# Kernel optimization log

Hardware: AMD Instinct MI355X
Metric: run time of the kernel (lower is better)

The kernel has to match this reference:

```python
import jax, jax.numpy as jnp
import numpy as np

B, T, N = 16, 16, 1024          # patients, max visits, code_num
C, G, H, A, P = 48, 32, 150, 32, 32  # code_size, graph_size, hidden_size, t_attention_size, pool attn size
OUT = 1
NEG = -1e30


def setup_inputs() -> dict:
    key = jax.random.key(0)
    ks = jax.random.split(key, 20)
    code_x = (jax.random.uniform(ks[0], (B, T, N)) < 0.2).astype(jnp.float32)
    neighbors = (jax.random.uniform(ks[1], (B, T, N)) < 0.2).astype(jnp.float32)
    cat = jax.random.randint(ks[2], (B, T, N), 0, 8)
    # divided[..., 0/1/2] = disjoint m1 (persistent) / m2 (emerging-neighbor) / m3 (emerging-unrelated) masks
    divided = jnp.stack([(cat == 0), (cat == 1), (cat == 2)], axis=-1).astype(jnp.int32)
    lens = jax.random.randint(ks[3], (B,), 1, T + 1)
    prior = jax.random.uniform(ks[4], (N,))
    adj = (jax.random.uniform(ks[5], (N, N)) * (jax.random.uniform(ks[6], (N, N)) < 0.05)).astype(jnp.float32)

    def nrm(k, shape, scale=0.05):
        return (jax.random.normal(k, shape) * scale).astype(jnp.float32)

    return dict(
        code_x=code_x, divided=divided, neighbors=neighbors, lens=lens, prior=prior, adj=adj,
        c_emb=nrm(ks[7], (N, C)), n_emb=nrm(ks[8], (N, C)), u_emb=nrm(ks[9], (N, G)),
        Wg=nrm(ks[10], (C, G)), bg=jnp.zeros((G,), jnp.float32),
        W_ih=nrm(ks[11], (3 * H, G)), b_ih=jnp.zeros((3 * H,), jnp.float32),
        W_hh=nrm(ks[12], (3 * H, H)), b_hh=jnp.zeros((3 * H,), jnp.float32),
        Wq=nrm(ks[13], (G, A)), bq=jnp.zeros((A,), jnp.float32),
        Wk=nrm(ks[14], (G, A)), bk=jnp.zeros((A,), jnp.float32),
        Wv=nrm(ks[15], (G, H)), bv=jnp.zeros((H,), jnp.float32),
        Wp=nrm(ks[16], (H, P)), bp=jnp.zeros((P,), jnp.float32),
        ctx=nrm(ks[17], (P,)),
        Wc=nrm(ks[18], (H, OUT)), bc=jnp.zeros((OUT,), jnp.float32),
    )


def _forward(code_x, divided, neighbors, lens, prior, adj, c_emb, n_emb, u_emb,
             Wg, bg, W_ih, b_ih, W_hh, b_hh, Wq, bq, Wk, bk, Wv, bv,
             Wp, bp, ctx, Wc, bc):
    pr = prior[:, None]                                  # [N,1] disease prior scaling of graph messages
    scale = 1.0 / jnp.sqrt(jnp.asarray(A, jnp.float32))

    def gru(x, h):
        # torch nn.GRUCell semantics; x: [B,N,G], h: [B,N,H]
        gi = jnp.einsum('bng,kg->bnk', x, W_ih) + b_ih
        gh = jnp.einsum('bnh,kh->bnk', h, W_hh) + b_hh
        ir, iz, i_n = jnp.split(gi, 3, -1)
        hr, hz, h_n = jnp.split(gh, 3, -1)
        r = jax.nn.sigmoid(ir + hr)
        z = jax.nn.sigmoid(iz + hz)
        cand = jnp.tanh(i_n + r * h_n)
        return (1.0 - z) * cand + z * h

    def step(carry, xs):
        h_prev, no_prev, t = carry
        cx, nb, dv = xs                                  # [B,N], [B,N], [B,N,3]
        c = cx[..., None]
        n = nb[..., None]
        # --- GraphLayer: adjacency message passing, prior-weighted ---
        ce = c * c_emb                                   # [B,N,C]
        ne = n * n_emb
        agg_c = jnp.einsum('mn,bnc->bmc', adj, ce) * pr
        agg_n = jnp.einsum('mn,bnc->bmc', adj, ne) * pr
        co = jax.nn.leaky_relu((ce + c * (agg_c + agg_n)) @ Wg + bg)   # [B,N,G]
        no = jax.nn.leaky_relu((ne + n * (agg_n + agg_c)) @ Wg + bg)
        # --- TransitionLayer ---
        m1 = dv[..., 0] > 0
        m2 = dv[..., 1] > 0
        m3 = dv[..., 2] > 0
        m23 = m2 | m3
        h_gru = gru(co, h_prev)                          # GRU branch for persistent codes (m1)
        # attention branch: queries = prev-step neighbor embeddings (m2) or unrelated embeddings (m3)
        qf = jnp.where(m2[..., None], no_prev, 0.0) + jnp.where(m3[..., None], u_emb, 0.0)
        q = qf @ Wq + bq
        k = co @ Wk + bk
        v = co @ Wv + bv                                 # [B,N,H]
        g = jnp.einsum('bma,bna->bmn', q, k) * scale     # scores over active m2|m3 keys only
        g = jnp.where(m23[:, None, :], g, NEG)
        h_att = jnp.tanh(jnp.einsum('bmn,bnh->bmh', jax.nn.softmax(g, axis=-1), v))
        t_pos = (t > 0).astype(co.dtype)                 # m23 branch only runs for t > 0 (as in original)
        h_new = jnp.where(m1[..., None], h_gru, 0.0) + t_pos * jnp.where(m23[..., None], h_att, 0.0)
        # masked maxes (0 when the index set is empty, as in original)
        om1 = jnp.max(jnp.where(m1[..., None], h_gru, NEG), axis=1)
        om1 = jnp.where(jnp.any(m1, axis=1)[:, None], om1, 0.0)
        om23 = jnp.max(jnp.where(m23[..., None], h_att, NEG), axis=1)
        om23 = jnp.where(jnp.any(m23, axis=1)[:, None], om23, 0.0)
        out_t = om1 + t_pos * om23                       # [B,H]
        return (h_new, no, t + 1), out_t

    h0 = jnp.zeros((B, N, H), jnp.float32)
    no0 = jnp.zeros((B, N, G), jnp.float32)
    xs = (jnp.transpose(code_x, (1, 0, 2)),
          jnp.transpose(neighbors, (1, 0, 2)),
          jnp.transpose(divided, (1, 0, 2, 3)))
    _, outs = jax.lax.scan(step, (h0, no0, jnp.int32(0)), xs)
    outs = jnp.transpose(outs, (1, 0, 2))                # [B,T,H]
    # --- DotProductAttention pooling over valid (ragged) timesteps ---
    vu = (outs @ Wp + bp) @ ctx                          # [B,T]
    valid = jnp.arange(T)[None, :] < lens[:, None]
    score = jax.nn.softmax(jnp.where(valid, vu, NEG), axis=-1)
    pooled = jnp.sum(outs * score[..., None], axis=1)    # [B,H]
    # --- Classifier (dropout identity at eval, activation=None) ---
    return pooled @ Wc + bc


def reference(code_x, divided, neighbors, lens, prior, adj, c_emb, n_emb, u_emb,
              Wg, bg, W_ih, b_ih, W_hh, b_hh, Wq, bq, Wk, bk, Wv, bv,
              Wp, bp, ctx, Wc, bc):
    return _forward(code_x, divided, neighbors, lens, prior, adj, c_emb, n_emb, u_emb,
                    Wg, bg, W_ih, b_ih, W_hh, b_hh, Wq, bq, Wk, bk, Wv, bv,
                    Wp, bp, ctx, Wc, bc)
```

## Files before the change

kernel.cpp:

```cpp
#include <hip/hip_runtime.h>

#define B_ 16
#define T_ 16
#define N_ 1024
#define C_ 48
#define G_ 32
#define H_ 150
#define A_ 32
#define P_ 32
#define H3_ 450
#define NNZ_CAP 262144
#define CAP1 256
#define CAP23 384
#define CHCAP 40960
#define CHCAPL 16384
#define SCALE_ 0.17677669529663687f

__device__ __forceinline__ unsigned fenc(float f){
  unsigned u = __float_as_uint(f);
  return (u & 0x80000000u) ? ~u : (u | 0x80000000u);
}
__device__ __forceinline__ float fdec(unsigned e){
  unsigned u = (e & 0x80000000u) ? (e & 0x7fffffffu) : ~e;
  return __uint_as_float(u);
}
__device__ __forceinline__ float sigmf(float x){ return 1.f/(1.f+__expf(-x)); }
__device__ __forceinline__ float wmaxf(float v){
  #pragma unroll
  for (int d=32; d>0; d>>=1) v = fmaxf(v, __shfl_xor(v,d));
  return v;
}

#define FMA16(W, PTR, ACC) do { \
    const float4* _c4 = (const float4*)(PTR); \
    float4 _c0=_c4[0], _c1=_c4[1], _c2=_c4[2], _c3=_c4[3]; \
    ACC[0]=fmaf((W),_c0.x,ACC[0]); ACC[1]=fmaf((W),_c0.y,ACC[1]); \
    ACC[2]=fmaf((W),_c0.z,ACC[2]); ACC[3]=fmaf((W),_c0.w,ACC[3]); \
    ACC[4]=fmaf((W),_c1.x,ACC[4]); ACC[5]=fmaf((W),_c1.y,ACC[5]); \
    ACC[6]=fmaf((W),_c1.z,ACC[6]); ACC[7]=fmaf((W),_c1.w,ACC[7]); \
    ACC[8]=fmaf((W),_c2.x,ACC[8]); ACC[9]=fmaf((W),_c2.y,ACC[9]); \
    ACC[10]=fmaf((W),_c2.z,ACC[10]); ACC[11]=fmaf((W),_c2.w,ACC[11]); \
    ACC[12]=fmaf((W),_c3.x,ACC[12]); ACC[13]=fmaf((W),_c3.y,ACC[13]); \
    ACC[14]=fmaf((W),_c3.z,ACC[14]); ACC[15]=fmaf((W),_c3.w,ACC[15]); \
  } while(0)

__global__ void k_csr_cnt(const float* __restrict__ adj, int* __restrict__ rcnt){
  int m = blockIdx.x; int tid = threadIdx.x;
  int c = 0;
  for (int n = tid; n < N_; n += 256) c += (adj[(size_t)m*N_+n] != 0.f) ? 1 : 0;
  __shared__ int sr[256];
  sr[tid]=c; __syncthreads();
  for (int s=128; s>0; s>>=1){ if (tid<s) sr[tid]+=sr[tid+s]; __syncthreads(); }
  if (tid==0) rcnt[m]=sr[0];
}
__global__ void k_csr_scan(const int* __restrict__ rcnt, int* __restrict__ rowptr){
  int lane = threadIdx.x;
  int s = 0;
  for (int r=0;r<16;++r) s += rcnt[lane*16+r];
  int incl = s;
  for (int d=1; d<64; d<<=1){ int y = __shfl_up(incl, d); if (lane>=d) incl += y; }
  int run = incl - s;
  for (int r=0;r<16;++r){ rowptr[lane*16+r] = run; run += rcnt[lane*16+r]; }
  if (lane==63) rowptr[N_] = incl;
}
__global__ void k_csr_fill(const float* __restrict__ adj, const float* __restrict__ prior,
                           const int* __restrict__ rowptr,
                           int* __restrict__ ccol, float* __restrict__ cval){
  int m = blockIdx.x; int lane = threadIdx.x;
  int base = rowptr[m];
  float pm = prior[m];
  for (int it=0; it<N_/64; ++it){
    int n = it*64+lane;
    float a = adj[(size_t)m*N_+n];
    bool pnz = (a != 0.f);
    unsigned long long mk = __ballot(pnz);
    if (pnz){
      int idx = base + __popcll(mk & ((1ULL<<lane)-1ULL));
      if (idx < NNZ_CAP){ ccol[idx]=n; cval[idx]=a*pm; }
    }
    base += __popcll(mk);
  }
}

__global__ void k_masks(const int* __restrict__ divided, int* __restrict__ lst23,
                        int* __restrict__ pos1,
                        int* __restrict__ cnt23, int* __restrict__ cnt1){
  int bt = blockIdx.x; int lane = threadIdx.x;
  int base23=0, base1=0;
  for (int it=0; it<N_/64; ++it){
    int n = it*64+lane;
    const int* dv = &divided[((size_t)bt*N_+n)*3];
    int d0=dv[0], d1=dv[1], d2=dv[2];
    bool p23 = (d1>0)||(d2>0); bool p1 = d0>0;
    unsigned long long mk23 = __ballot(p23);
    unsigned long long mk1  = __ballot(p1);
    unsigned long long ltm = (1ULL<<lane)-1ULL;
    if (p23){ int idx = base23 + __popcll(mk23 & ltm); lst23[(size_t)bt*N_+idx]=n; }
    if (p1){ int idx = base1 + __popcll(mk1 & ltm); pos1[(size_t)bt*N_+n]=idx; }
    base23 += __popcll(mk23); base1 += __popcll(mk1);
  }
  if (lane==0){ cnt23[bt]=base23; cnt1[bt]=base1; }
}

__global__ void k_chains(const int* __restrict__ divided,
                         unsigned* __restrict__ chN, int* __restrict__ nchN,
                         unsigned* __restrict__ chH, int* __restrict__ nchH,
                         unsigned* __restrict__ chL, int* __restrict__ nchL){
  int idx = blockIdx.x*256 + threadIdx.x;
  if (idx >= B_*N_) return;
  int b = idx >> 10, n = idx & (N_-1);
  unsigned m1m = 0;
  for (int t=0;t<T_;++t){
    int d0 = divided[(((size_t)(b*T_+t))*N_ + n)*3];
    if (d0>0) m1m |= (1u<<t);
  }
  unsigned heads = m1m & ~(m1m<<1);
  while (heads){
    int t0 = __builtin_ctz(heads); heads &= (heads-1u);
    unsigned run = m1m >> t0;
    int len = __builtin_ctz(~run);
    unsigned enc = ((unsigned)b<<18)|((unsigned)n<<8)|((unsigned)t0<<4)|(unsigned)(len-1);
    int f = 0;
    if (t0 >= 2){
      size_t pidx = ((size_t)(b*T_+t0-1)*N_ + n)*3;
      if ((divided[pidx+1] | divided[pidx+2]) > 0) f = 1;
    }
    if (f){ int i2 = atomicAdd(nchH,1); if (i2 < CHCAP) chH[i2]=enc; }
    else  { int i2 = atomicAdd(nchN,1); if (i2 < CHCAP) chN[i2]=enc; }
    if (len >= 2){
      int i2 = atomicAdd(nchL, 1);
      if (i2 < CHCAPL) chL[i2] = enc;
    }
  }
}

__global__ void k_wt(const float* __restrict__ W_ih, const float* __restrict__ W_hh,
                     const float* __restrict__ Wq, const float* __restrict__ bq,
                     const float* __restrict__ Wk,
                     float* __restrict__ WihT, float* __restrict__ WhhT,
                     float* __restrict__ Md){
  int idx = blockIdx.x*256+threadIdx.x;
  if (idx < G_*H3_){ int g=idx/H3_, k=idx-g*H3_; WihT[g*H3_+k]=W_ih[(size_t)k*G_+g]; }
  int idx2 = idx - G_*H3_;
  if (idx2>=0 && idx2 < H_*H3_){ int h=idx2/H3_, k=idx2-h*H3_; WhhT[h*H3_+k]=W_hh[(size_t)k*H_+h]; }
  int e = idx - (G_*H3_ + H_*H3_);
  if (e>=0 && e<1024){
    int g=e>>5, gp=e&31;
    float acc=0.f;
    #pragma unroll
    for (int a=0;a<A_;++a) acc = fmaf(Wq[g*A_+a], Wk[gp*A_+a], acc);
    Md[e]=acc;
  }
  int e2 = e - 1024;
  if (e2>=0 && e2<32){
    float acc=0.f;
    #pragma unroll
    for (int a=0;a<A_;++a) acc = fmaf(Wk[e2*A_+a], bq[a], acc);
    Md[1024+e2]=acc;
  }
}

__global__ void k_init(float* __restrict__ om23f, int* __restrict__ nchN,
                       int* __restrict__ nchH, int* __restrict__ nchL){
  int i = blockIdx.x*256+threadIdx.x;
  if (i<B_*T_*H_){ om23f[i]=0.f; }
  if (i==0){ *nchN = 0; *nchH = 0; *nchL = 0; }
}

__global__ __launch_bounds__(256) void k_cono(
    const float* __restrict__ code_x, const float* __restrict__ neighbors,
    const int* __restrict__ divided,
    const int* __restrict__ rowptr, const int* __restrict__ ccol, const float* __restrict__ cval,
    const float* __restrict__ c_emb, const float* __restrict__ n_emb,
    const float* __restrict__ Wg, const float* __restrict__ bg,
    float* __restrict__ co, float* __restrict__ no_)
{
  __shared__ float sCo[4][C_], sNo[4][C_];
  int w = threadIdx.x >> 6, lane = threadIdx.x & 63;
  int gw = blockIdx.x*4 + w;
  int bt = gw >> 10, m = gw & (N_-1);
  int t = bt & (T_-1);
  const int* dv = &divided[(size_t)gw*3];
  int d0=dv[0], d1=dv[1], d2=dv[2];
  bool needCo = (d0|d1|d2) > 0;
  bool needNo = (t < T_-1) && (divided[((size_t)(gw+N_))*3+1] > 0);
  if (!needCo && !needNo) return;
  float cxm = code_x[gw], nbm = neighbors[gw];
  float acc = 0.f;
  bool needAcc = (needCo && cxm!=0.f) || (needNo && nbm!=0.f);
  if (needAcc){
    int s = rowptr[m], e = rowptr[m+1];
    if (s > NNZ_CAP) s = NNZ_CAP;
    if (e > NNZ_CAP) e = NNZ_CAP;
    int btN = bt << 10;
    for (int base = s; base < e; base += 64){
      int j = base + lane;
      int cc = 0; float wx = 0.f, wy = 0.f;
      if (j < e){
        cc = ccol[j];
        float cv = cval[j];
        float xs = code_x[btN+cc], ys = neighbors[btN+cc];
        wx = cv*xs; wy = cv*ys;
      }
      unsigned long long mk = __ballot(wx!=0.f || wy!=0.f);
      while (mk){
        int u0 = __builtin_ctzll(mk); mk &= (mk-1ULL);
        int u1 = -1;
        if (mk){ u1 = __builtin_ctzll(mk); mk &= (mk-1ULL); }
        int u1s = (u1>=0)? u1 : u0;
        int n0 = __shfl(cc,u0); float a0x=__shfl(wx,u0), a0y=__shfl(wy,u0);
        int n1 = __shfl(cc,u1s); float a1x=__shfl(wx,u1s), a1y=__shfl(wy,u1s);
        float ce0=0.f,ne0=0.f,ce1=0.f,ne1=0.f;
        if (lane < C_){
          ce0 = c_emb[(size_t)n0*C_+lane]; ne0 = n_emb[(size_t)n0*C_+lane];
          ce1 = c_emb[(size_t)n1*C_+lane]; ne1 = n_emb[(size_t)n1*C_+lane];
        }
        acc = fmaf(a0x, ce0, acc); acc = fmaf(a0y, ne0, acc);
        if (u1>=0){ acc = fmaf(a1x, ce1, acc); acc = fmaf(a1y, ne1, acc); }
      }
    }
  }
  if (lane < C_){
    sCo[w][lane] = cxm * (c_emb[(size_t)m*C_+lane] + acc);
    sNo[w][lane] = nbm * (n_emb[(size_t)m*C_+lane] + acc);
  }
  asm volatile("s_waitcnt lgkmcnt(0)" ::: "memory");
  int g = lane & 31; bool isNo = lane >= 32;
  const float* src = isNo ? sNo[w] : sCo[w];
  float a2 = bg[g];
  #pragma unroll
  for (int c=0;c<C_;++c) a2 = fmaf(src[c], Wg[c*G_+g], a2);
  float r = a2 >= 0.f ? a2 : 0.01f*a2;
  if (isNo ? needNo : needCo){
    float* dst = isNo ? no_ : co;
    dst[(size_t)gw*G_ + g] = r;
  }
}

__global__ __launch_bounds__(384) void k_attn(
    const float* __restrict__ co, const float* __restrict__ no_,
    const float* __restrict__ u_emb, const int* __restrict__ divided,
    const int* __restrict__ lst23, const int* __restrict__ cnt23, const int* __restrict__ pos1,
    const float* __restrict__ Md, const float* __restrict__ Wv, const float* __restrict__ bv,
    float* __restrict__ hsel, float* __restrict__ om23f)
{
  int b = blockIdx.x; int t = blockIdx.y + 1; int bt = b*T_ + t;
  int cnt = cnt23[bt]; if (cnt > CAP23) cnt = CAP23;
  if (cnt == 0) return;
  __shared__ int   sLst[CAP23];
  __shared__ __align__(16) float sCo[CAP23][G_];
  __shared__ __align__(16) float sW[G_*H_ + H_ + 8];
  __shared__ unsigned sMax[H_];
  int tid = threadIdx.x; int lane = tid & 63;
  for (int i=tid; i<cnt; i+=384) sLst[i] = lst23[(size_t)bt*N_+i];
  for (int i=tid; i<1056; i+=384) sW[i] = Md[i];
  unsigned sent = fenc(-1e30f);
  for (int i=tid; i<H_; i+=384) sMax[i] = sent;
  __syncthreads();
  for (int i=tid; i<cnt*8; i+=384){
    int rrow = i>>3, seg = i&7;
    float4 v = *(const float4*)&co[((((size_t)bt<<10) + sLst[rrow])<<5) + seg*4];
    *(float4*)&sCo[rrow][seg*4] = v;
  }
  bool act = (tid < cnt);
  int n = 0;
  float qpp[G_];
  if (act){
    n = sLst[tid];
    int d1 = divided[((size_t)bt*N_+n)*3+1];
    const float* qsrc = (d1>0) ? &no_[((((size_t)(bt-1))<<10)+n)<<5] : &u_emb[(size_t)n*G_];
    float4 qv[8];
    #pragma unroll
    for (int j=0;j<8;++j) qv[j] = ((const float4*)qsrc)[j];
    #pragma unroll
    for (int j=0;j<G_;++j) qpp[j] = sW[1024+j];
    #pragma unroll
    for (int g=0; g<G_; ++g){
      float qfg = (g&3)==0 ? qv[g>>2].x : (g&3)==1 ? qv[g>>2].y : (g&3)==2 ? qv[g>>2].z : qv[g>>2].w;
      const float4* mr = (const float4*)&sW[g*G_];
      #pragma unroll
      for (int j=0;j<8;++j){
        float4 mj = mr[j];
        qpp[4*j+0] = fmaf(qfg, mj.x, qpp[4*j+0]);
        qpp[4*j+1] = fmaf(qfg, mj.y, qpp[4*j+1]);
        qpp[4*j+2] = fmaf(qfg, mj.z, qpp[4*j+2]);
        qpp[4*j+3] = fmaf(qfg, mj.w, qpp[4*j+3]);
      }
    }
  } else {
    #pragma unroll
    for (int j=0;j<G_;++j) qpp[j]=0.f;
  }
  __syncthreads();
  for (int i=tid; i<G_*H_; i+=384){
    int h=i>>5, g=i&31;
    sW[h*G_+g] = Wv[(size_t)g*H_+h];
  }
  for (int i=tid; i<H_; i+=384) sW[G_*H_+i] = bv[i];
  float pbar[G_]; float l = 0.f;
  #pragma unroll
  for (int j=0;j<G_;++j) pbar[j]=0.f;
  if (act){
    #pragma unroll 2
    for (int c=0;c<cnt;++c){
      const float4* col = (const float4*)&sCo[c][0];
      float4 xv[8];
      #pragma unroll
      for (int j=0;j<8;++j) xv[j]=col[j];
      float d0=0.f,d1v=0.f,d2v=0.f,d3=0.f;
      #pragma unroll
      for (int j=0;j<8;j+=4){
        d0 = fmaf(qpp[4*j+0], xv[j].x, d0); d1v = fmaf(qpp[4*j+1], xv[j].y, d1v);
        d2v = fmaf(qpp[4*j+2], xv[j].z, d2v); d3 = fmaf(qpp[4*j+3], xv[j].w, d3);
        d0 = fmaf(qpp[4*j+4], xv[j+1].x, d0); d1v = fmaf(qpp[4*j+5], xv[j+1].y, d1v);
        d2v = fmaf(qpp[4*j+6], xv[j+1].z, d2v); d3 = fmaf(qpp[4*j+7], xv[j+1].w, d3);
        d0 = fmaf(qpp[4*j+8], xv[j+2].x, d0); d1v = fmaf(qpp[4*j+9], xv[j+2].y, d1v);
        d2v = fmaf(qpp[4*j+10], xv[j+2].z, d2v); d3 = fmaf(qpp[4*j+11], xv[j+2].w, d3);
        d0 = fmaf(qpp[4*j+12], xv[j+3].x, d0); d1v = fmaf(qpp[4*j+13], xv[j+3].y, d1v);
        d2v = fmaf(qpp[4*j+14], xv[j+3].z, d2v); d3 = fmaf(qpp[4*j+15], xv[j+3].w, d3);
      }
      float dot = (d0+d1v)+(d2v+d3);
      float pv = __expf(dot*SCALE_);
      l += pv;
      #pragma unroll
      for (int j=0;j<8;++j){
        pbar[4*j+0] = fmaf(pv, xv[j].x, pbar[4*j+0]);
        pbar[4*j+1] = fmaf(pv, xv[j].y, pbar[4*j+1]);
        pbar[4*j+2] = fmaf(pv, xv[j].z, pbar[4*j+2]);
        pbar[4*j+3] = fmaf(pv, xv[j].w, pbar[4*j+3]);
      }
    }
  }
  if (!act) l = 1.f;
  float inv = 1.f/l;
  #pragma unroll
  for (int j=0;j<G_;++j) pbar[j]*=inv;
  __syncthreads();
  bool wsel=false; float* hd=nullptr;
  if (act && t+1 < T_){
    size_t nidx = ((size_t)b*T_+(t+1))*N_ + n;
    if (divided[nidx*3+0] > 0){
      int pos = pos1[nidx];
      if (pos >= 0 && pos < CAP1){ wsel=true; hd=&hsel[(((size_t)b*T_+t)*CAP1 + pos)*H_]; }
    }
  }
  for (int h=0; h<H_; ++h){
    float acc = sW[G_*H_+h];
    const float4* wv = (const float4*)&sW[h*G_];
    #pragma unroll
    for (int j=0;j<8;++j){
      float4 wj = wv[j];
      acc = fmaf(pbar[4*j+0], wj.x, acc);
      acc = fmaf(pbar[4*j+1], wj.y, acc);
      acc = fmaf(pbar[4*j+2], wj.z, acc);
      acc = fmaf(pbar[4*j+3], wj.w, acc);
    }
    float o = act ? tanhf(acc) : -1e30f;
    float om = wmaxf(o);
    if (lane==0) atomicMax(&sMax[h], fenc(om));
    if (wsel) hd[h] = o;
  }
  __syncthreads();
  for (int i=tid; i<H_; i+=384) om23f[(size_t)bt*H_+i] = fdec(sMax[i]);
}

__global__ __launch_bounds__(256) void k_gruheadN(
    const float* __restrict__ co, const int* __restrict__ pos1,
    const unsigned* __restrict__ chN, const int* __restrict__ nchN,
    const float* __restrict__ WihT, const float* __restrict__ b_ih,
    const float* __restrict__ b_hh, float* __restrict__ gout)
{
  __shared__ __align__(16) float sCoT[G_][16];
  __shared__ float sG[16][452];
  __shared__ int sBt[16], sN[16], sPos[16];
  int tid = threadIdx.x;
  int NC = *nchN; if (NC > CHCAP) NC = CHCAP;
  int base = blockIdx.x * 16;
  if (base >= NC) return;
  int num = min(16, NC - base);
  if (tid < 16){
    if (tid < num){
      unsigned cl = chN[base+tid];
      int b = cl>>18, n = (cl>>8)&1023, t0 = (cl>>4)&15;
      int bt = b*T_ + t0;
      sBt[tid]=bt; sN[tid]=n; sPos[tid]=pos1[(size_t)bt*N_+n];
    } else { sBt[tid]=0; sN[tid]=0; sPos[tid]=-1; }
  }
  __syncthreads();
  for (int i=tid; i<G_*16; i+=256){
    int g = i>>4, ii = i&15;
    sCoT[g][ii] = (ii<num) ? co[((size_t)sBt[ii]*N_+sN[ii])*G_+g] : 0.f;
  }
  __syncthreads();
  for (int pass=0; pass<2; ++pass){
    int k = pass*256 + tid;
    if (k < H3_){
      float acc[16];
      #pragma unroll
      for (int u=0;u<16;++u) acc[u]=0.f;
      for (int g=0; g<G_; ++g){
        float wih = WihT[g*H3_ + k];
        FMA16(wih, &sCoT[g][0], acc);
      }
      #pragma unroll
      for (int u=0;u<16;++u) sG[u][k] = acc[u];
    }
  }
  __syncthreads();
  for (int i=tid; i<num*152; i+=256){
    int s = i/152, h = i - s*152;
    if (h < H_){
      int pos = sPos[s];
      if (pos >= 0 && pos < CAP1){
        float r = sigmf(sG[s][h]       + b_ih[h]       + b_hh[h]);
        float z = sigmf(sG[s][h+H_]    + b_ih[h+H_]    + b_hh[h+H_]);
        float cand = tanhf(sG[s][h+2*H_] + b_ih[h+2*H_] + r*b_hh[h+2*H_]);
        gout[((size_t)sBt[s]*CAP1 + pos)*H_ + h] = (1.f-z)*cand;
      }
    }
  }
}

__global__ __launch_bounds__(256) void k_gruheadH(
    const float* __restrict__ co, const float* __restrict__ hsel,
    const int* __restrict__ pos1,
    const unsigned* __restrict__ chH, const int* __restrict__ nchH,
    const float* __restrict__ WihT, const float* __restrict__ b_ih,
    const float* __restrict__ WhhT, const float* __restrict__ b_hh,
    float* __restrict__ gout)
{
  __shared__ __align__(16) float sCoT[G_][16];
  __shared__ __align__(16) float sHT[152][16];
  __shared__ float sG[16][452];
  __shared__ float sGhn[16][152];
  __shared__ int sBt[16], sN[16], sPos[16], sHo[16];
  int tid = threadIdx.x;
  int NC = *nchH; if (NC > CHCAP) NC = CHCAP;
  int base = blockIdx.x * 16;
  if (base >= NC) return;
  int num = min(16, NC - base);
  if (tid < 16){
    if (tid < num){
      unsigned cl = chH[base+tid];
      int b = cl>>18, n = (cl>>8)&1023, t0 = (cl>>4)&15;
      int bt = b*T_ + t0;
      int pos = pos1[(size_t)bt*N_+n];
      sBt[tid]=bt; sN[tid]=n; sPos[tid]=pos;
      sHo[tid] = (b*T_ + (t0-1))*CAP1 + ((pos>=0 && pos<CAP1) ? pos : 0);
    } else { sBt[tid]=0; sN[tid]=0; sPos[tid]=-1; sHo[tid]=0; }
  }
  __syncthreads();
  for (int i=tid; i<G_*16; i+=256){
    int g = i>>4, ii = i&15;
    sCoT[g][ii] = (ii<num) ? co[((size_t)sBt[ii]*N_+sN[ii])*G_+g] : 0.f;
  }
  for (int i=tid; i<152*16; i+=256){
    int q = i>>4, ii = i&15;
    float v = 0.f;
    if (ii < num && q < H_) v = hsel[(size_t)sHo[ii]*H_ + q];
    sHT[q][ii] = v;
  }
  __syncthreads();
  for (int pass=0; pass<2; ++pass){
    int k = pass*256 + tid;
    if (k < H3_){
      float acc[16];
      #pragma unroll
      for (int u=0;u<16;++u) acc[u]=0.f;
      for (int g=0; g<G_; ++g){
        float wih = WihT[g*H3_ + k];
        FMA16(wih, &sCoT[g][0], acc);
      }
      #pragma unroll
      for (int u=0;u<16;++u) sG[u][k] = acc[u];
    }
  }
  for (int pass=0; pass<2; ++pass){
    int k = pass*256 + tid;
    if (k < H3_){
      float acc[16];
      #pragma unroll
      for (int u=0;u<16;++u) acc[u]=0.f;
      for (int q=0; q<H_; ++q){
        float whh = WhhT[q*H3_ + k];
        FMA16(whh, &sHT[q][0], acc);
      }
      if (k < 2*H_){
        #pragma unroll
        for (int u=0;u<16;++u) sG[u][k] += acc[u];
      } else {
        #pragma unroll
        for (int u=0;u<16;++u) sGhn[u][k-2*H_] = acc[u];
      }
    }
  }
  __syncthreads();
  for (int i=tid; i<num*152; i+=256){
    int s = i/152, h = i - s*152;
    if (h < H_){
      int pos = sPos[s];
      if (pos >= 0 && pos < CAP1){
        float hv = sHT[h][s];
        float r = sigmf(sG[s][h]       + b_ih[h]       + b_hh[h]);
        float z = sigmf(sG[s][h+H_]    + b_ih[h+H_]    + b_hh[h+H_]);
        float cand = tanhf(sG[s][h+2*H_] + b_ih[h+2*H_] + r*(sGhn[s][h] + b_hh[h+2*H_]));
        float o = (1.f-z)*cand + z*hv;
        gout[((size_t)sBt[s]*CAP1 + pos)*H_ + h] = o;
      }
    }
  }
}

__global__ __launch_bounds__(256) void k_grutail(
    const float* __restrict__ co, const int* __restrict__ pos1,
    const unsigned* __restrict__ chainsL, const int* __restrict__ nchL,
    const float* __restrict__ WihT, const float* __restrict__ b_ih,
    const float* __restrict__ WhhT, const float* __restrict__ b_hh,
    float* __restrict__ gout)
{
  __shared__ float hst[4][4][H_];
  int w = threadIdx.x >> 6, lane = threadIdx.x & 63;
  int NC = *nchL; if (NC > CHCAPL) NC = CHCAPL;
  int cbase = (blockIdx.x*4 + w)*4;
  if (cbase >= NC) return;

  int cbv[4], cnv[4], t0v[4], lenv[4];
  #pragma unroll
  for (int u=0;u<4;++u){
    int cid = cbase+u; bool ca = cid < NC;
    unsigned cl = chainsL[ca ? cid : (NC-1)];
    cbv[u]=cl>>18; cnv[u]=(cl>>8)&1023; t0v[u]=(cl>>4)&15;
    lenv[u]= ca ? (int)((cl&15)+1) : 1;
  }
  int maxlen = lenv[0];
  #pragma unroll
  for (int u=1;u<4;++u) maxlen = max(maxlen, lenv[u]);

  int h0=lane,h1=lane+64,h2=lane+128; bool has2=(h2<H_); int h2c=has2?h2:0;
  float bi[9], bh[9];
  bi[0]=b_ih[h0]; bi[1]=b_ih[h0+H_]; bi[2]=b_ih[h0+2*H_];
  bi[3]=b_ih[h1]; bi[4]=b_ih[h1+H_]; bi[5]=b_ih[h1+2*H_];
  bi[6]=b_ih[h2c]; bi[7]=b_ih[h2c+H_]; bi[8]=b_ih[h2c+2*H_];
  bh[0]=b_hh[h0]; bh[1]=b_hh[h0+H_]; bh[2]=b_hh[h0+2*H_];
  bh[3]=b_hh[h1]; bh[4]=b_hh[h1+H_]; bh[5]=b_hh[h1+2*H_];
  bh[6]=b_hh[h2c]; bh[7]=b_hh[h2c+H_]; bh[8]=b_hh[h2c+2*H_];

  for (int s=1; s<maxlen; ++s){
    bool as[4]; int btv[4];
    const float* hp[4];
    #pragma unroll
    for (int u=0;u<4;++u){
      as[u] = s < lenv[u];
      int t = t0v[u] + (as[u] ? s : 0);
      btv[u] = cbv[u]*T_ + t;
      if (s == 1 && as[u]){
        int btp = btv[u] - 1;
        int posp = pos1[(size_t)btp*N_ + cnv[u]];
        if (posp < 0 || posp >= CAP1) posp = 0;
        hp[u] = &gout[((size_t)btp*CAP1 + posp)*H_];
      } else {
        hp[u] = &hst[w][u][0];
      }
    }
    float gi[4][9], gh[4][9];
    #pragma unroll
    for (int u=0;u<4;++u){
      #pragma unroll
      for (int j=0;j<9;++j){ gi[u][j]=bi[j]; gh[u][j]=bh[j]; }
    }
    const float* cop[4];
    #pragma unroll
    for (int u=0;u<4;++u) cop[u] = &co[((size_t)btv[u]*N_ + cnv[u])*G_];
    for (int g=0; g<G_; ++g){
      const float* wr = &WihT[g*H3_];
      float wv[9];
      wv[0]=wr[h0]; wv[1]=wr[h0+H_]; wv[2]=wr[h0+2*H_];
      wv[3]=wr[h1]; wv[4]=wr[h1+H_]; wv[5]=wr[h1+2*H_];
      wv[6]=wr[h2c]; wv[7]=wr[h2c+H_]; wv[8]=wr[h2c+2*H_];
      #pragma unroll
      for (int u=0;u<4;++u){
        float cg = cop[u][g];
        #pragma unroll
        for (int j=0;j<9;++j) gi[u][j]=fmaf(cg, wv[j], gi[u][j]);
      }
    }
    for (int q=0;q<H_;++q){
      const float* wr=&WhhT[q*H3_];
      float wv[9];
      wv[0]=wr[h0]; wv[1]=wr[h0+H_]; wv[2]=wr[h0+2*H_];
      wv[3]=wr[h1]; wv[4]=wr[h1+H_]; wv[5]=wr[h1+2*H_];
      wv[6]=wr[h2c]; wv[7]=wr[h2c+H_]; wv[8]=wr[h2c+2*H_];
      #pragma unroll
      for (int u=0;u<4;++u){
        float hv = hp[u][q];
        #pragma unroll
        for (int j=0;j<9;++j) gh[u][j]=fmaf(hv, wv[j], gh[u][j]);
      }
    }
    #pragma unroll
    for (int u=0;u<4;++u){
      if (as[u]){
        float hv0 = hp[u][h0];
        float hv1 = hp[u][h1];
        float hv2 = has2 ? hp[u][h2] : 0.f;
        float r0=sigmf(gi[u][0]+gh[u][0]), z0=sigmf(gi[u][1]+gh[u][1]);
        float cd0=tanhf(gi[u][2]+r0*gh[u][2]);
        float o0=(1.f-z0)*cd0 + z0*hv0;
        float r1=sigmf(gi[u][3]+gh[u][3]), z1=sigmf(gi[u][4]+gh[u][4]);
        float cd1=tanhf(gi[u][5]+r1*gh[u][5]);
        float o1=(1.f-z1)*cd1 + z1*hv1;
        float o2=0.f;
        if (has2){
          float r2=sigmf(gi[u][6]+gh[u][6]), z2=sigmf(gi[u][7]+gh[u][7]);
          float cd2=tanhf(gi[u][8]+r2*gh[u][8]);
          o2=(1.f-z2)*cd2 + z2*hv2;
        }
        float* hd = &hst[w][u][0];
        hd[h0]=o0; hd[h1]=o1; if (has2) hd[h2]=o2;
        int pos = pos1[(size_t)btv[u]*N_ + cnv[u]];
        if (pos >= 0 && pos < CAP1){
          float* gd = &gout[((size_t)btv[u]*CAP1 + pos)*H_];
          gd[h0]=o0; gd[h1]=o1; if (has2) gd[h2]=o2;
        }
      }
    }
    asm volatile("s_waitcnt lgkmcnt(0)" ::: "memory");
  }
}

__global__ __launch_bounds__(256) void k_om1(
    const float* __restrict__ gout, const int* __restrict__ cnt1, float* __restrict__ om1f)
{
  int bt = blockIdx.x; int tid = threadIdx.x;
  int c1 = cnt1[bt]; if (c1 > CAP1) c1 = CAP1;
  if (tid < H_){
    float mx = -1e30f;
    for (int r=0;r<c1;++r) mx = fmaxf(mx, gout[((size_t)bt*CAP1+r)*H_+tid]);
    om1f[(size_t)bt*H_+tid] = (c1>0) ? mx : 0.f;
  }
}

__global__ __launch_bounds__(256) void k_final(
    const float* __restrict__ om1f, const float* __restrict__ om23f,
    const float* __restrict__ Wp, const float* __restrict__ bp,
    const float* __restrict__ ctx, const float* __restrict__ Wc, const float* __restrict__ bc,
    const int* __restrict__ lens, float* __restrict__ out)
{
  int b = blockIdx.x; int tid = threadIdx.x;
  __shared__ float sOut[T_][H_];
  __shared__ float sTP[T_][P_];
  __shared__ float sVu[T_], sSc[T_], sPool[H_];
  __shared__ float sRed[256];
  for (int i=tid; i<T_*H_; i+=256){
    int t=i/H_, h=i-t*H_;
    float o1 = om1f[((size_t)b*T_+t)*H_+h];
    float o2 = (t>0)? om23f[((size_t)b*T_+t)*H_+h] : 0.f;
    sOut[t][h]=o1+o2;
  }
  __syncthreads();
  for (int pr = tid; pr < T_*P_; pr += 256){
    int t = pr / P_, p = pr - t*P_;
    float acc = bp[p];
    for (int h=0;h<H_;++h) acc = fmaf(sOut[t][h], Wp[h*P_+p], acc);
    sTP[t][p] = acc * ctx[p];
  }
  __syncthreads();
  if (tid < T_){
    float v=0.f;
    for (int p=0;p<P_;++p) v += sTP[tid][p];
    sVu[tid]=v;
  }
  __syncthreads();
  if (tid==0){
    int L = lens[b]; if (L<1) L=1; if (L>T_) L=T_;
    float mx=-1e30f;
    for (int t=0;t<L;++t) mx = fmaxf(mx, sVu[t]);
    float s=0.f;
    for (int t=0;t<L;++t){ float e=__expf(sVu[t]-mx); sSc[t]=e; s+=e; }
    float inv=1.f/s;
    for (int t=0;t<T_;++t) sSc[t] = (t<L)? sSc[t]*inv : 0.f;
  }
  __syncthreads();
  if (tid < H_){
    float acc=0.f;
    for (int t=0;t<T_;++t) acc = fmaf(sOut[t][tid], sSc[t], acc);
    sPool[tid]=acc;
  }
  __syncthreads();
  float v = (tid<H_)? sPool[tid]*Wc[tid] : 0.f;
  sRed[tid]=v; __syncthreads();
  for (int s=128;s>0;s>>=1){ if (tid<s) sRed[tid]+=sRed[tid+s]; __syncthreads(); }
  if (tid==0) out[b] = sRed[0] + bc[0];
}

extern "C" void kernel_launch(void* const* d_in, const int* in_sizes, int n_in,
                              void* d_out, int out_size, void* d_ws, size_t ws_size,
                              hipStream_t stream)
{
  const float* code_x=(const float*)d_in[0];
  const int*   divided=(const int*)d_in[1];
  const float* neighbors=(const float*)d_in[2];
  const int*   lens=(const int*)d_in[3];
  const float* prior=(const float*)d_in[4];
  const float* adj=(const float*)d_in[5];
  const float* c_emb=(const float*)d_in[6];
  const float* n_emb=(const float*)d_in[7];
  const float* u_emb=(const float*)d_in[8];
  const float* Wg=(const float*)d_in[9];
  const float* bg=(const float*)d_in[10];
  const float* W_ih=(const float*)d_in[11];
  const float* b_ih=(const float*)d_in[12];
  const float* W_hh=(const float*)d_in[13];
  const float* b_hh=(const float*)d_in[14];
  const float* Wq=(const float*)d_in[15];
  const float* bq=(const float*)d_in[16];
  const float* Wk=(const float*)d_in[17];
  const float* bk=(const float*)d_in[18];
  const float* Wv=(const float*)d_in[19];
  const float* bv=(const float*)d_in[20];
  const float* Wp=(const float*)d_in[21];
  const float* bp=(const float*)d_in[22];
  const float* ctx=(const float*)d_in[23];
  const float* Wc=(const float*)d_in[24];
  const float* bc=(const float*)d_in[25];
  float* out=(float*)d_out;
  (void)in_sizes; (void)n_in; (void)out_size; (void)ws_size; (void)bk;

  char* p=(char*)d_ws;
  size_t off=0;
  auto carve=[&](size_t bytes)->char*{ char* r=p+off; off=(off+bytes+255)&~(size_t)255; return r; };
  int*   rowptr=(int*)carve((N_+1)*4);
  int*   rcnt  =(int*)carve(N_*4);
  int*   ccol  =(int*)carve((size_t)NNZ_CAP*4);
  float* cval  =(float*)carve((size_t)NNZ_CAP*4);
  int*   cnt23 =(int*)carve(B_*T_*4);
  int*   cnt1  =(int*)carve(B_*T_*4);
  int*   lst23 =(int*)carve((size_t)B_*T_*N_*4);
  int*   pos1  =(int*)carve((size_t)B_*T_*N_*4);
  float* co    =(float*)carve((size_t)B_*T_*N_*G_*4);
  float* no_   =(float*)carve((size_t)B_*T_*N_*G_*4);
  float* WihT  =(float*)carve((size_t)G_*H3_*4);
  float* WhhT  =(float*)carve((size_t)H_*H3_*4);
  float* Md    =(float*)carve(1056*4);
  float* hsel  =(float*)carve((size_t)B_*T_*CAP1*H_*4);
  float* gout  =(float*)carve((size_t)B_*T_*CAP1*H_*4);
  unsigned* chainsN=(unsigned*)carve((size_t)CHCAP*4);
  unsigned* chainsH=(unsigned*)carve((size_t)CHCAP*4);
  unsigned* chainsL=(unsigned*)carve((size_t)CHCAPL*4);
  int*   nchN  =(int*)carve(256);
  int*   nchH  =(int*)carve(256);
  int*   nchL  =(int*)carve(256);
  float* om1f  =(float*)carve((size_t)B_*T_*H_*4);
  float* om23f =(float*)carve((size_t)B_*T_*H_*4);

  k_csr_cnt<<<N_,256,0,stream>>>(adj, rcnt);
  k_csr_scan<<<1,64,0,stream>>>(rcnt, rowptr);
  k_csr_fill<<<N_,64,0,stream>>>(adj, prior, rowptr, ccol, cval);
  k_masks<<<B_*T_,64,0,stream>>>(divided, lst23, pos1, cnt23, cnt1);
  k_wt<<<325,256,0,stream>>>(W_ih, W_hh, Wq, bq, Wk, WihT, WhhT, Md);
  k_init<<<(B_*T_*H_+255)/256,256,0,stream>>>(om23f, nchN, nchH, nchL);
  k_chains<<<(B_*N_+255)/256,256,0,stream>>>(divided, chainsN, nchN, chainsH, nchH, chainsL, nchL);
  k_cono<<<B_*T_*N_/4,256,0,stream>>>(code_x, neighbors, divided, rowptr, ccol, cval,
                                      c_emb, n_emb, Wg, bg, co, no_);
  k_attn<<<dim3(B_, T_-1),384,0,stream>>>(co, no_, u_emb, divided,
                                      lst23, cnt23, pos1, Md, Wv, bv,
                                      hsel, om23f);
  k_gruheadN<<<CHCAP/16,256,0,stream>>>(co, pos1, chainsN, nchN,
                                      WihT, b_ih, b_hh, gout);
  k_gruheadH<<<CHCAP/16,256,0,stream>>>(co, hsel, pos1, chainsH, nchH,
                                      WihT, b_ih, WhhT, b_hh, gout);
  k_grutail<<<CHCAPL/16,256,0,stream>>>(co, pos1, chainsL, nchL,
                                      WihT, b_ih, WhhT, b_hh, gout);
  k_om1<<<B_*T_,256,0,stream>>>(gout, cnt1, om1f);
  k_final<<<B_,256,0,stream>>>(om1f, om23f, Wp,bp,ctx,Wc,bc, lens, out);
}
```

Measured before the change: 525.7 us.

## Split attention key range across two thread groups and move Wv transpose upstream

The attention kernel now launches 768 threads per (batch, visit) block. Two 384-thread groups each process half of the key columns for the same queries, and their partial softmax numerators and denominators are combined through shared memory. The Wv transpose moves into the weight-prep kernel, and Md and WvT are read from global memory instead of being staged in shared memory, which frees LDS. The output projection is split so each group computes 75 of the 150 hidden units. This roughly halves the serial per-thread loop in a kernel launched as only 240 blocks, at the cost of extra barriers and global-memory (cache) reads of the weights.

```diff
diff --git a/kernel.cpp b/kernel.cpp
--- a/kernel.cpp
+++ b/kernel.cpp
@@ -136,9 +136,9 @@
 
 __global__ void k_wt(const float* __restrict__ W_ih, const float* __restrict__ W_hh,
                      const float* __restrict__ Wq, const float* __restrict__ bq,
-                     const float* __restrict__ Wk,
+                     const float* __restrict__ Wk, const float* __restrict__ Wv,
                      float* __restrict__ WihT, float* __restrict__ WhhT,
-                     float* __restrict__ Md){
+                     float* __restrict__ Md, float* __restrict__ WvT){
   int idx = blockIdx.x*256+threadIdx.x;
   if (idx < G_*H3_){ int g=idx/H3_, k=idx-g*H3_; WihT[g*H3_+k]=W_ih[(size_t)k*G_+g]; }
   int idx2 = idx - G_*H3_;
@@ -157,6 +157,11 @@
     #pragma unroll
     for (int a=0;a<A_;++a) acc = fmaf(Wk[e2*A_+a], bq[a], acc);
     Md[1024+e2]=acc;
+  }
+  int e3 = e - 1056;
+  if (e3>=0 && e3 < H_*G_){
+    int h = e3>>5, g = e3&31;
+    WvT[e3] = Wv[(size_t)g*H_+h];
   }
 }
 
@@ -237,11 +242,11 @@
   }
 }
 
-__global__ __launch_bounds__(384) void k_attn(
+__global__ __launch_bounds__(768) void k_attn(
     const float* __restrict__ co, const float* __restrict__ no_,
     const float* __restrict__ u_emb, const int* __restrict__ divided,
     const int* __restrict__ lst23, const int* __restrict__ cnt23, const int* __restrict__ pos1,
-    const float* __restrict__ Md, const float* __restrict__ Wv, const float* __restrict__ bv,
+    const float* __restrict__ Md, const float* __restrict__ WvT, const float* __restrict__ bv,
     float* __restrict__ hsel, float* __restrict__ om23f)
 {
   int b = blockIdx.x; int t = blockIdx.y + 1; int bt = b*T_ + t;
@@ -249,35 +254,36 @@
   if (cnt == 0) return;
   __shared__ int   sLst[CAP23];
   __shared__ __align__(16) float sCo[CAP23][G_];
-  __shared__ __align__(16) float sW[G_*H_ + H_ + 8];
+  __shared__ float sL[CAP23];
   __shared__ unsigned sMax[H_];
-  int tid = threadIdx.x; int lane = tid & 63;
-  for (int i=tid; i<cnt; i+=384) sLst[i] = lst23[(size_t)bt*N_+i];
-  for (int i=tid; i<1056; i+=384) sW[i] = Md[i];
+  int tid = threadIdx.x;
+  int grp = (tid >= 384) ? 1 : 0;
+  int r   = tid - 384*grp;
   unsigned sent = fenc(-1e30f);
-  for (int i=tid; i<H_; i+=384) sMax[i] = sent;
-  __syncthreads();
-  for (int i=tid; i<cnt*8; i+=384){
+  for (int i=tid; i<cnt; i+=768) sLst[i] = lst23[(size_t)bt*N_+i];
+  for (int i=tid; i<H_; i+=768) sMax[i] = sent;
+  __syncthreads();
+  for (int i=tid; i<cnt*8; i+=768){
     int rrow = i>>3, seg = i&7;
     float4 v = *(const float4*)&co[((((size_t)bt<<10) + sLst[rrow])<<5) + seg*4];
     *(float4*)&sCo[rrow][seg*4] = v;
   }
-  bool act = (tid < cnt);
+  bool act = (r < cnt);
   int n = 0;
   float qpp[G_];
   if (act){
-    n = sLst[tid];
+    n = sLst[r];
     int d1 = divided[((size_t)bt*N_+n)*3+1];
     const float* qsrc = (d1>0) ? &no_[((((size_t)(bt-1))<<10)+n)<<5] : &u_emb[(size_t)n*G_];
     float4 qv[8];
     #pragma unroll
     for (int j=0;j<8;++j) qv[j] = ((const float4*)qsrc)[j];
     #pragma unroll
-    for (int j=0;j<G_;++j) qpp[j] = sW[1024+j];
+    for (int j=0;j<G_;++j) qpp[j] = Md[1024+j];
     #pragma unroll
     for (int g=0; g<G_; ++g){
       float qfg = (g&3)==0 ? qv[g>>2].x : (g&3)==1 ? qv[g>>2].y : (g&3)==2 ? qv[g>>2].z : qv[g>>2].w;
-      const float4* mr = (const float4*)&sW[g*G_];
+      const float4* mr = (const float4*)&Md[g*G_];
       #pragma unroll
       for (int j=0;j<8;++j){
         float4 mj = mr[j];
@@ -292,17 +298,15 @@
     for (int j=0;j<G_;++j) qpp[j]=0.f;
   }
   __syncthreads();
-  for (int i=tid; i<G_*H_; i+=384){
-    int h=i>>5, g=i&31;
-    sW[h*G_+g] = Wv[(size_t)g*H_+h];
-  }
-  for (int i=tid; i<H_; i+=384) sW[G_*H_+i] = bv[i];
+  int half = (cnt+1)>>1;
+  int c0 = grp ? half : 0;
+  int c1 = grp ? cnt  : half;
   float pbar[G_]; float l = 0.f;
   #pragma unroll
   for (int j=0;j<G_;++j) pbar[j]=0.f;
   if (act){
     #pragma unroll 2
-    for (int c=0;c<cnt;++c){
+    for (int c=c0;c<c1;++c){
       const float4* col = (const float4*)&sCo[c][0];
       float4 xv[8];
       #pragma unroll
@@ -331,11 +335,32 @@
       }
     }
   }
-  if (!act) l = 1.f;
-  float inv = 1.f/l;
-  #pragma unroll
-  for (int j=0;j<G_;++j) pbar[j]*=inv;
-  __syncthreads();
+  __syncthreads();
+  if (act && grp==0){
+    #pragma unroll
+    for (int j=0;j<G_;++j) sCo[r][j] = pbar[j];
+    sL[r] = l;
+  }
+  __syncthreads();
+  if (act && grp==1){
+    #pragma unroll
+    for (int j=0;j<G_;++j) sCo[r][j] += pbar[j];
+    sL[r] += l;
+  }
+  __syncthreads();
+  float pb[G_];
+  if (act){
+    float inv = 1.f / sL[r];
+    const float4* pr = (const float4*)&sCo[r][0];
+    #pragma unroll
+    for (int j=0;j<8;++j){
+      float4 pv4 = pr[j];
+      pb[4*j+0]=pv4.x*inv; pb[4*j+1]=pv4.y*inv; pb[4*j+2]=pv4.z*inv; pb[4*j+3]=pv4.w*inv;
+    }
+  } else {
+    #pragma unroll
+    for (int j=0;j<G_;++j) pb[j]=0.f;
+  }
   bool wsel=false; float* hd=nullptr;
   if (act && t+1 < T_){
     size_t nidx = ((size_t)b*T_+(t+1))*N_ + n;
@@ -344,16 +369,18 @@
       if (pos >= 0 && pos < CAP1){ wsel=true; hd=&hsel[(((size_t)b*T_+t)*CAP1 + pos)*H_]; }
     }
   }
-  for (int h=0; h<H_; ++h){
-    float acc = sW[G_*H_+h];
-    const float4* wv = (const float4*)&sW[h*G_];
+  int lane = tid & 63;
+  int hA = grp*75, hB = hA + 75;
+  for (int h=hA; h<hB; ++h){
+    float acc = bv[h];
+    const float4* wr = (const float4*)&WvT[h*G_];
     #pragma unroll
     for (int j=0;j<8;++j){
-      float4 wj = wv[j];
-      acc = fmaf(pbar[4*j+0], wj.x, acc);
-      acc = fmaf(pbar[4*j+1], wj.y, acc);
-      acc = fmaf(pbar[4*j+2], wj.z, acc);
-      acc = fmaf(pbar[4*j+3], wj.w, acc);
+      float4 wj = wr[j];
+      acc = fmaf(pb[4*j+0], wj.x, acc);
+      acc = fmaf(pb[4*j+1], wj.y, acc);
+      acc = fmaf(pb[4*j+2], wj.z, acc);
+      acc = fmaf(pb[4*j+3], wj.w, acc);
     }
     float o = act ? tanhf(acc) : -1e30f;
     float om = wmaxf(o);
@@ -361,7 +388,7 @@
     if (wsel) hd[h] = o;
   }
   __syncthreads();
-  for (int i=tid; i<H_; i+=384) om23f[(size_t)bt*H_+i] = fdec(sMax[i]);
+  for (int i=tid; i<H_; i+=768) om23f[(size_t)bt*H_+i] = fdec(sMax[i]);
 }
 
 __global__ __launch_bounds__(256) void k_gruheadN(
@@ -742,6 +769,7 @@
   float* WihT  =(float*)carve((size_t)G_*H3_*4);
   float* WhhT  =(float*)carve((size_t)H_*H3_*4);
   float* Md    =(float*)carve(1056*4);
+  float* WvT   =(float*)carve((size_t)H_*G_*4);
   float* hsel  =(float*)carve((size_t)B_*T_*CAP1*H_*4);
   float* gout  =(float*)carve((size_t)B_*T_*CAP1*H_*4);
   unsigned* chainsN=(unsigned*)carve((size_t)CHCAP*4);
@@ -757,13 +785,13 @@
   k_csr_scan<<<1,64,0,stream>>>(rcnt, rowptr);
   k_csr_fill<<<N_,64,0,stream>>>(adj, prior, rowptr, ccol, cval);
   k_masks<<<B_*T_,64,0,stream>>>(divided, lst23, pos1, cnt23, cnt1);
-  k_wt<<<325,256,0,stream>>>(W_ih, W_hh, Wq, bq, Wk, WihT, WhhT, Md);
+  k_wt<<<343,256,0,stream>>>(W_ih, W_hh, Wq, bq, Wk, Wv, WihT, WhhT, Md, WvT);
   k_init<<<(B_*T_*H_+255)/256,256,0,stream>>>(om23f, nchN, nchH, nchL);
   k_chains<<<(B_*N_+255)/256,256,0,stream>>>(divided, chainsN, nchN, chainsH, nchH, chainsL, nchL);
   k_cono<<<B_*T_*N_/4,256,0,stream>>>(code_x, neighbors, divided, rowptr, ccol, cval,
                                       c_emb, n_emb, Wg, bg, co, no_);
-  k_attn<<<dim3(B_, T_-1),384,0,stream>>>(co, no_, u_emb, divided,
-                                      lst23, cnt23, pos1, Md, Wv, bv,
+  k_attn<<<dim3(B_, T_-1),768,0,stream>>>(co, no_, u_emb, divided,
+                                      lst23, cnt23, pos1, Md, WvT, bv,
                                       hsel, om23f);
   k_gruheadN<<<CHCAP/16,256,0,stream>>>(co, pos1, chainsN, nchN,
                                       WihT, b_ih, b_hh, gout);
```

Measured after the change: 479.0 us. 1.1x faster.
